# Kernel tuning notes

Measured on AMD Instinct MI355X. Metric: run time of the kernel, lower is better.

The kernel has to match this reference:

```python
import jax, jax.numpy as jnp
import numpy as np

B = 4096        # batch
KD = 64         # koopman_dim
NC = 24         # complex eigenvalue pairs
NR = 16         # real eigenvalues (KD = 2*NC + NR)
DT = 0.01       # delta_t
LC = 2 * NC     # complex net latent/out dim
LR = NR         # real net latent/out dim


def setup_inputs() -> dict:
    key = jax.random.key(0)
    ks = jax.random.split(key, 9)
    def w(k, o, i):
        return jax.random.normal(k, (o, i), dtype=jnp.float32) / np.sqrt(i)
    return {
        "x": jax.random.normal(ks[0], (B, 1, KD), dtype=jnp.float32),
        "Wc1": w(ks[1], LC, KD), "bc1": jnp.zeros((LC,), jnp.float32),
        "Wc2": w(ks[2], LC, LC), "bc2": jnp.zeros((LC,), jnp.float32),
        "Wr1": w(ks[3], LR, KD), "br1": jnp.zeros((LR,), jnp.float32),
        "Wr2": w(ks[4], LR, LR), "br2": jnp.zeros((LR,), jnp.float32),
        "T": 256,
    }


def reference(x, Wc1, bc1, Wc2, bc2, Wr1, br1, Wr2, br2, T):
    # Sequential Koopman rollout. Instead of materializing the [B,KD,KD]
    # block-diagonal K each step, apply the 2x2 rotation*decay blocks and the
    # real decay directly (identical math, no dense matmul).
    dt = jnp.float32(DT)

    def step(y, _):
        # complex parametrization MLP: [B,KD] -> [B,2*NC]
        co = jnp.tanh(y @ Wc1.T + bc1) @ Wc2.T + bc2
        co = co.reshape(-1, NC, 2)
        mu, omega = co[..., 0], co[..., 1]          # [B,NC] each
        scale = jnp.exp(dt * mu)
        c = jnp.cos(dt * omega) * scale             # cos*exp
        s = jnp.sin(dt * omega) * scale             # sin*exp
        yc = y[:, :2 * NC].reshape(-1, NC, 2)       # paired complex coords
        new_c = jnp.stack(
            [c * yc[..., 0] - s * yc[..., 1],
             s * yc[..., 0] + c * yc[..., 1]], axis=-1
        ).reshape(-1, 2 * NC)
        # real parametrization MLP: [B,KD] -> [B,NR]
        re = jnp.tanh(y @ Wr1.T + br1) @ Wr2.T + br2
        new_r = jnp.exp(dt * re) * y[:, 2 * NC:]
        y_new = jnp.concatenate([new_c, new_r], axis=-1)
        return y_new, y_new

    y0 = x[:, 0, :]
    _, Ys = jax.lax.scan(step, y0, None, length=T)  # [T,B,KD]
    return jnp.swapaxes(Ys, 0, 1)                   # [B,T,KD]
```

## Files before the change

### kernel.cpp

```cpp
#include <hip/hip_runtime.h>

#define NB    4096
#define TSTEP 256
#define EPB   16
#define DTC   0.01f

typedef _Float16 h8 __attribute__((ext_vector_type(8)));
typedef _Float16 h4 __attribute__((ext_vector_type(4)));
typedef float    f4 __attribute__((ext_vector_type(4)));

#define KE  0.014426950409f
#define REV 1.59154943e-3f

__device__ __forceinline__ float fast_tanh(float a) {
    float t = fminf(a * 2.885390082f, 126.0f);
    float E = __builtin_amdgcn_exp2f(t);
    return (E - 1.0f) * __builtin_amdgcn_rcpf(E + 1.0f);
}

#define U16B  2304
#define Y32B  4608

__global__ void __launch_bounds__(256)
koopman_kernel(const float* __restrict__ x,
               const float* __restrict__ Wc1, const float* __restrict__ bc1,
               const float* __restrict__ Wc2, const float* __restrict__ bc2,
               const float* __restrict__ Wr1, const float* __restrict__ br1,
               const float* __restrict__ Wr2, const float* __restrict__ br2,
               float* __restrict__ out)
{
    const int tid  = threadIdx.x;
    const int lane = tid & 63;
    const int w    = tid >> 6;
    const int blk  = blockIdx.x;

    __shared__ __align__(16) unsigned char L[Y32B + 16*272];

    const int e = lane & 15;
    const int g = lane >> 4;

    const int fa = 16*w + e;
    h8 a1lo, a1hi, a2lo, a2hi;
    {
        const float* r1 = (fa < 48) ? (Wc1 + fa*64) : (Wr1 + (fa-48)*64);
        #pragma unroll
        for (int i = 0; i < 8; ++i) {
            a1lo[i] = (_Float16)r1[8*g + i];
            a1hi[i] = (_Float16)r1[32 + 8*g + i];
        }
        #pragma unroll
        for (int i = 0; i < 8; ++i) {
            const int k0 = 8*g + i, k1 = k0 + 32;
            float v0, v1;
            if (fa < 48) {
                v0 = (k0 < 48) ? Wc2[fa*48 + k0] : 0.0f;
                v1 = (k1 < 48) ? Wc2[fa*48 + k1] : 0.0f;
            } else {
                v0 = (k0 >= 48) ? Wr2[(fa-48)*16 + (k0-48)] : 0.0f;
                v1 = (k1 >= 48) ? Wr2[(fa-48)*16 + (k1-48)] : 0.0f;
            }
            a2lo[i] = (_Float16)v0;
            a2hi[i] = (_Float16)v1;
        }
    }
    float b1v[4], b2v[4], ys[4];
    #pragma unroll
    for (int r = 0; r < 4; ++r) {
        const int f = 16*w + 4*g + r;
        b1v[r] = (f < 48) ? bc1[f] : br1[f-48];
        b2v[r] = (f < 48) ? bc2[f] : br2[f-48];
        ys[r]  = x[(blk*EPB + e)*64 + f];
    }
    const bool cwave = (w < 3);

    const int rdoff  = e*144 + 16*g;
    const int wroff  = e*144 + (16*w + 4*g)*2;
    const int w32off = Y32B + e*272 + (16*w + 4*g)*4;
    const int sel = tid >> 4, sf4 = (tid & 15)*4;
    const int stoff = Y32B + sel*272 + sf4*4;
    float* gp = out + (size_t)(blk*EPB + sel) * (TSTEP*64) + sf4;

    {
        const f4 xv = *reinterpret_cast<const f4*>(x + (blk*EPB + sel)*64 + sf4);
        h4 p; p[0]=(_Float16)xv[0]; p[1]=(_Float16)xv[1]; p[2]=(_Float16)xv[2]; p[3]=(_Float16)xv[3];
        *reinterpret_cast<h4*>(L + sel*144 + sf4*2) = p;
    }
    __syncthreads();

    for (int t = 0; t < TSTEP; ++t) {
        const h8 by0 = *reinterpret_cast<const h8*>(L + rdoff);
        const h8 by1 = *reinterpret_cast<const h8*>(L + rdoff + 64);
        f4 a = {b1v[0], b1v[1], b1v[2], b1v[3]};
        a = __builtin_amdgcn_mfma_f32_16x16x32_f16(a1lo, by0, a, 0, 0, 0);
        a = __builtin_amdgcn_mfma_f32_16x16x32_f16(a1hi, by1, a, 0, 0, 0);
        h4 up;
        up[0]=(_Float16)fast_tanh(a[0]); up[1]=(_Float16)fast_tanh(a[1]);
        up[2]=(_Float16)fast_tanh(a[2]); up[3]=(_Float16)fast_tanh(a[3]);
        *reinterpret_cast<h4*>(L + U16B + wroff) = up;
        __syncthreads();

        const h8 bu0 = *reinterpret_cast<const h8*>(L + U16B + rdoff);
        const h8 bu1 = *reinterpret_cast<const h8*>(L + U16B + rdoff + 64);
        f4 c = {b2v[0], b2v[1], b2v[2], b2v[3]};
        c = __builtin_amdgcn_mfma_f32_16x16x32_f16(a2lo, bu0, c, 0, 0, 0);
        c = __builtin_amdgcn_mfma_f32_16x16x32_f16(a2hi, bu1, c, 0, 0, 0);

        if (cwave) {
            const float sc0 = __builtin_amdgcn_exp2f(KE * c[0]);
            const float sc1 = __builtin_amdgcn_exp2f(KE * c[2]);
            const float s0 = __builtin_amdgcn_sinf(REV * c[1]) * sc0;
            const float c0 = __builtin_amdgcn_cosf(REV * c[1]) * sc0;
            const float s1 = __builtin_amdgcn_sinf(REV * c[3]) * sc1;
            const float c1 = __builtin_amdgcn_cosf(REV * c[3]) * sc1;
            const float n0 = c0*ys[0] - s0*ys[1];
            const float n1 = s0*ys[0] + c0*ys[1];
            const float n2 = c1*ys[2] - s1*ys[3];
            const float n3 = s1*ys[2] + c1*ys[3];
            ys[0]=n0; ys[1]=n1; ys[2]=n2; ys[3]=n3;
        } else {
            ys[0] *= __builtin_amdgcn_exp2f(KE * c[0]);
            ys[1] *= __builtin_amdgcn_exp2f(KE * c[1]);
            ys[2] *= __builtin_amdgcn_exp2f(KE * c[2]);
            ys[3] *= __builtin_amdgcn_exp2f(KE * c[3]);
        }

        h4 yp;
        yp[0]=(_Float16)ys[0]; yp[1]=(_Float16)ys[1]; yp[2]=(_Float16)ys[2]; yp[3]=(_Float16)ys[3];
        *reinterpret_cast<h4*>(L + wroff) = yp;
        f4 yv = {ys[0], ys[1], ys[2], ys[3]};
        *reinterpret_cast<f4*>(L + w32off) = yv;
        __syncthreads();

        const f4 sv = *reinterpret_cast<const f4*>(L + stoff);
        *reinterpret_cast<f4*>(gp) = sv;
        gp += 64;
    }
}

extern "C" void kernel_launch(void* const* d_in, const int* in_sizes, int n_in,
                              void* d_out, int out_size, void* d_ws, size_t ws_size,
                              hipStream_t stream) {
    const float* x   = (const float*)d_in[0];
    const float* Wc1 = (const float*)d_in[1];
    const float* bc1 = (const float*)d_in[2];
    const float* Wc2 = (const float*)d_in[3];
    const float* bc2 = (const float*)d_in[4];
    const float* Wr1 = (const float*)d_in[5];
    const float* br1 = (const float*)d_in[6];
    const float* Wr2 = (const float*)d_in[7];
    const float* br2 = (const float*)d_in[8];
    float* out = (float*)d_out;

    koopman_kernel<<<dim3(NB / EPB), dim3(256), 0, stream>>>(
        x, Wc1, bc1, Wc2, bc2, Wr1, br1, Wr2, br2, out);
}
```

Measured before the change: 123.2 us.

## Store outputs directly from registers and use LDS-only barriers with split MFMA chains

Drops the fp32 LDS staging buffer for outputs and has each thread write its own four floats straight to global memory. That removes one LDS store, one LDS read and the barrier between them on every step. __syncthreads is replaced with a barrier that waits only on LDS counters, so outstanding global stores do not stall the loop. The dependent MFMA pairs are split into two independent accumulators that are summed afterwards, shortening the dependency chain. The trade-off is less coalesced global writes (16-byte pieces with a stride per row) and a barrier that relies on a hand-written waitcnt.

```diff
diff --git a/kernel.cpp b/kernel.cpp
--- a/kernel.cpp
+++ b/kernel.cpp
@@ -18,8 +18,13 @@
     return (E - 1.0f) * __builtin_amdgcn_rcpf(E + 1.0f);
 }
 
+__device__ __forceinline__ void lds_barrier() {
+    asm volatile("s_waitcnt lgkmcnt(0)" ::: "memory");
+    __builtin_amdgcn_s_barrier();
+    asm volatile("" ::: "memory");
+}
+
 #define U16B  2304
-#define Y32B  4608
 
 __global__ void __launch_bounds__(256)
 koopman_kernel(const float* __restrict__ x,
@@ -34,7 +39,7 @@
     const int w    = tid >> 6;
     const int blk  = blockIdx.x;
 
-    __shared__ __align__(16) unsigned char L[Y32B + 16*272];
+    __shared__ __align__(16) unsigned char L[U16B * 2];
 
     const int e = lane & 15;
     const int g = lane >> 4;
@@ -73,37 +78,39 @@
     }
     const bool cwave = (w < 3);
 
-    const int rdoff  = e*144 + 16*g;
-    const int wroff  = e*144 + (16*w + 4*g)*2;
-    const int w32off = Y32B + e*272 + (16*w + 4*g)*4;
-    const int sel = tid >> 4, sf4 = (tid & 15)*4;
-    const int stoff = Y32B + sel*272 + sf4*4;
-    float* gp = out + (size_t)(blk*EPB + sel) * (TSTEP*64) + sf4;
+    const int rdoff = e*144 + 16*g;
+    const int wroff = e*144 + (16*w + 4*g)*2;
+    float* gp = out + (size_t)(blk*EPB + e) * (TSTEP*64) + 16*w + 4*g;
 
     {
-        const f4 xv = *reinterpret_cast<const f4*>(x + (blk*EPB + sel)*64 + sf4);
+        const int row = tid >> 4, col4 = (tid & 15) * 4;
+        const f4 xv = *reinterpret_cast<const f4*>(x + (blk*EPB + row)*64 + col4);
         h4 p; p[0]=(_Float16)xv[0]; p[1]=(_Float16)xv[1]; p[2]=(_Float16)xv[2]; p[3]=(_Float16)xv[3];
-        *reinterpret_cast<h4*>(L + sel*144 + sf4*2) = p;
+        *reinterpret_cast<h4*>(L + row*144 + col4*2) = p;
     }
     __syncthreads();
 
     for (int t = 0; t < TSTEP; ++t) {
         const h8 by0 = *reinterpret_cast<const h8*>(L + rdoff);
         const h8 by1 = *reinterpret_cast<const h8*>(L + rdoff + 64);
-        f4 a = {b1v[0], b1v[1], b1v[2], b1v[3]};
-        a = __builtin_amdgcn_mfma_f32_16x16x32_f16(a1lo, by0, a, 0, 0, 0);
-        a = __builtin_amdgcn_mfma_f32_16x16x32_f16(a1hi, by1, a, 0, 0, 0);
+        f4 aL = {b1v[0], b1v[1], b1v[2], b1v[3]};
+        f4 aH = {0.0f, 0.0f, 0.0f, 0.0f};
+        aL = __builtin_amdgcn_mfma_f32_16x16x32_f16(a1lo, by0, aL, 0, 0, 0);
+        aH = __builtin_amdgcn_mfma_f32_16x16x32_f16(a1hi, by1, aH, 0, 0, 0);
+        const f4 a = aL + aH;
         h4 up;
         up[0]=(_Float16)fast_tanh(a[0]); up[1]=(_Float16)fast_tanh(a[1]);
         up[2]=(_Float16)fast_tanh(a[2]); up[3]=(_Float16)fast_tanh(a[3]);
         *reinterpret_cast<h4*>(L + U16B + wroff) = up;
-        __syncthreads();
+        lds_barrier();
 
         const h8 bu0 = *reinterpret_cast<const h8*>(L + U16B + rdoff);
         const h8 bu1 = *reinterpret_cast<const h8*>(L + U16B + rdoff + 64);
-        f4 c = {b2v[0], b2v[1], b2v[2], b2v[3]};
-        c = __builtin_amdgcn_mfma_f32_16x16x32_f16(a2lo, bu0, c, 0, 0, 0);
-        c = __builtin_amdgcn_mfma_f32_16x16x32_f16(a2hi, bu1, c, 0, 0, 0);
+        f4 cL = {b2v[0], b2v[1], b2v[2], b2v[3]};
+        f4 cH = {0.0f, 0.0f, 0.0f, 0.0f};
+        cL = __builtin_amdgcn_mfma_f32_16x16x32_f16(a2lo, bu0, cL, 0, 0, 0);
+        cH = __builtin_amdgcn_mfma_f32_16x16x32_f16(a2hi, bu1, cH, 0, 0, 0);
+        const f4 c = cL + cH;
 
         if (cwave) {
             const float sc0 = __builtin_amdgcn_exp2f(KE * c[0]);
@@ -128,12 +135,9 @@
         yp[0]=(_Float16)ys[0]; yp[1]=(_Float16)ys[1]; yp[2]=(_Float16)ys[2]; yp[3]=(_Float16)ys[3];
         *reinterpret_cast<h4*>(L + wroff) = yp;
         f4 yv = {ys[0], ys[1], ys[2], ys[3]};
-        *reinterpret_cast<f4*>(L + w32off) = yv;
-        __syncthreads();
-
-        const f4 sv = *reinterpret_cast<const f4*>(L + stoff);
-        *reinterpret_cast<f4*>(gp) = sv;
+        *reinterpret_cast<f4*>(gp) = yv;
         gp += 64;
+        lds_barrier();
     }
 }
 
```

After: 122.5 us (median of 2 runs). About the same (-0.6%).
